# Performance work log

Hardware: AMD Instinct MI355X
Metric: run time of the kernel (lower is better)

The kernel has to match this reference:

```python
import jax, jax.numpy as jnp
import numpy as np

MARGIN = 1.0  # init kwarg
BIG = 1e9     # finite sentinel for masked reductions (dist in [0, 2])


def setup_inputs() -> dict:
    key = jax.random.key(0)
    k1, k2 = jax.random.split(key)
    embeddings = jax.random.normal(k1, (8192, 256), dtype=jnp.float32)
    labels = jax.random.randint(k2, (8192,), 0, 128)
    return {"embeddings": embeddings, "labels": labels}


def reference(embeddings, labels):
    # cosine distance matrix: 1 - x_hat @ x_hat^T, clamped at 0
    norm = jnp.linalg.norm(embeddings, axis=1, keepdims=True)
    x = embeddings / jnp.maximum(norm, 1e-12)  # matches F.normalize eps
    dist = jnp.clip(1.0 - x @ x.T, 0.0, None)  # (B, B)

    same = labels[:, None] == labels[None, :]
    eye = jnp.eye(labels.shape[0], dtype=bool)
    pos_mask = same & ~eye   # same label, different index
    neg_mask = ~same         # different label

    # hard mining: hardest positive (max dist), hardest negative (min dist)
    pos_dist = jnp.max(jnp.where(pos_mask, dist, -BIG), axis=1)  # (B,)
    neg_dist = jnp.min(jnp.where(neg_mask, dist, BIG), axis=1)   # (B,)

    valid = pos_mask.any(axis=1) & neg_mask.any(axis=1)          # (B,)
    per_anchor = jnp.maximum(pos_dist - neg_dist + MARGIN, 0.0)
    loss_sum = jnp.sum(jnp.where(valid, per_anchor, 0.0))
    count = jnp.sum(valid).astype(dist.dtype)
    return jnp.where(count > 0, loss_sum / jnp.maximum(count, 1.0), 0.0)
```

## Files before the change

kernel.cpp:

```cpp
#include <hip/hip_runtime.h>
#include <hip/hip_bf16.h>


constexpr int NB = 8192;
constexpr int NBT = NB / 128;
constexpr int NBLK = NBT * (NBT + 1) / 2;

typedef __attribute__((ext_vector_type(8))) short bf16x8;
typedef __attribute__((ext_vector_type(4))) float f32x4;

typedef __attribute__((address_space(3))) unsigned int lds_u32;
typedef __attribute__((address_space(1))) const unsigned int g_u32;

__device__ inline void load_lds16(const unsigned short* g, unsigned short* l) {
    __builtin_amdgcn_global_load_lds((g_u32*)g, (lds_u32*)l, 16, 0, 0);
}

__device__ inline unsigned short f2bf(float v) {
    __hip_bfloat16 b = __float2bfloat16(v);
    return *reinterpret_cast<unsigned short*>(&b);
}

#define ENC6 0x40C00000u

__global__ __launch_bounds__(256) void norm_kernel(const float* __restrict__ X,
                                                   unsigned short* __restrict__ Xbt,
                                                   unsigned int* minKey,
                                                   unsigned int* maxKey) {
    __shared__ float tile[32][260];
    __shared__ float psum[32][8];
    __shared__ float rscale[32];
    const int t = threadIdx.x;
    const int rb = blockIdx.x * 32;
    const int g = blockIdx.x * 256 + t;
    if (g < NB) { minKey[g] = 0xFFFFFFFFu; maxKey[g] = 0u; }
    #pragma unroll
    for (int k = 0; k < 8; k++) {
        const int f = k * 256 + t;
        const int row = f >> 6, c4 = f & 63;
        const float4 v = *((const float4*)(X + (size_t)(rb + row) * 256) + c4);
        *(float4*)&tile[row][c4 * 4] = v;
    }
    __syncthreads();
    {
        const int r = t >> 3, e = t & 7;
        float s = 0.f;
        #pragma unroll
        for (int i = 0; i < 32; i++) { const float v = tile[r][e * 32 + i]; s += v * v; }
        psum[r][e] = s;
    }
    __syncthreads();
    if (t < 32) {
        float s = 0.f;
        #pragma unroll
        for (int e = 0; e < 8; e++) s += psum[t][e];
        rscale[t] = 1.0f / fmaxf(sqrtf(s), 1e-12f);
    }
    __syncthreads();
    #pragma unroll
    for (int j = 0; j < 4; j++) {
        const int idx = j * 256 + t;
        const int q = idx >> 5, r = idx & 31;
        const float sc = rscale[r];
        unsigned short tmp[8];
        #pragma unroll
        for (int e = 0; e < 8; e++) tmp[e] = f2bf(tile[r][q * 8 + e] * sc);
        *(bf16x8*)(Xbt + ((size_t)q * NB + rb + r) * 8) = *(bf16x8*)tmp;
    }
}

__global__ __launch_bounds__(256) void mine_kernel(
    const unsigned short* __restrict__ Xbt, const int* __restrict__ labels,
    unsigned int* minKey, unsigned int* maxKey) {
    __shared__ unsigned short Bt[32 * 512];
    __shared__ float Lrow[128], Lcol[128];

    const int tb = blockIdx.x;
    int a = (int)((sqrtf(8.0f * (float)tb + 1.0f) - 1.0f) * 0.5f);
    while ((a + 1) * (a + 2) / 2 <= tb) a++;
    while (a * (a + 1) / 2 > tb) a--;
    const int Iblk = tb - a * (a + 1) / 2;
    const int Jblk = a;
    const bool isdiag = (Iblk == Jblk);
    const int Irow0 = Iblk * 128;
    const int Jcol0 = Jblk * 128;

    const int tid = threadIdx.x;
    const int w = tid >> 6;
    const int lane = tid & 63;
    const int quad = lane >> 4;
    const int l16 = lane & 15;
    const int h = w & 1;
    const int v = w >> 1;

    if (tid < 128) Lrow[tid] = (float)labels[Irow0 + tid];
    else Lcol[tid - 128] = (float)labels[Jcol0 + tid - 128];

    f32x4 acc[4][4];
    #pragma unroll
    for (int mi = 0; mi < 4; mi++)
        #pragma unroll
        for (int ni = 0; ni < 4; ni++) acc[mi][ni] = (f32x4){0.f, 0.f, 0.f, 0.f};

    for (int kb = 0; kb < 4; kb++) {
        __syncthreads();
        #pragma unroll
        for (int s = 0; s < 8; s++) {
            const int rg = w * 8 + s;
            const int r2 = rg & 15;
            const int ks = r2 >> 3;
            const int ti = r2 & 7;
            const int base = (rg >> 4) ? Jcol0 : Irow0;
            const int c = kb * 8 + ks * 4 + (lane >> 4);
            const size_t u = (size_t)c * NB + base + ti * 16 + l16;
            load_lds16(Xbt + u * 8, Bt + rg * 512);
        }
        __syncthreads();

        #pragma unroll
        for (int ks = 0; ks < 2; ks++) {
            bf16x8 af[4], bf[4];
            #pragma unroll
            for (int i = 0; i < 4; i++) {
                af[i] = *(const bf16x8*)(Bt + (ks * 8 + h * 4 + i) * 512 + lane * 8);
                bf[i] = *(const bf16x8*)(Bt + (16 + ks * 8 + v * 4 + i) * 512 + lane * 8);
            }
            #pragma unroll
            for (int mi = 0; mi < 4; mi++)
                #pragma unroll
                for (int ni = 0; ni < 4; ni++)
                    acc[mi][ni] = __builtin_amdgcn_mfma_f32_16x16x32_bf16(
                        af[mi], bf[ni], acc[mi][ni], 0, 0, 0);
        }
    }

    const bool diagwave = isdiag && (h == v);
    float flc[4], cMin[4], cMax[4];
    #pragma unroll
    for (int ni = 0; ni < 4; ni++) {
        flc[ni] = Lcol[v * 64 + ni * 16 + l16];
        cMin[ni] = 1e30f;
        cMax[ni] = -1e30f;
    }
    #pragma unroll
    for (int mi = 0; mi < 4; mi++)
        #pragma unroll
        for (int r = 0; r < 4; r++) {
            const float flr = Lrow[h * 64 + mi * 16 + quad * 4 + r];
            float rMin = 1e30f, rMax = -1e30f;
            #pragma unroll
            for (int ni = 0; ni < 4; ni++) {
                const float uu = fminf(fabsf(flr - flc[ni]), 1.0f);
                float key = fmaf(uu, 8.0f, acc[mi][ni][r]);
                if (diagwave && mi == ni)
                    key = (l16 == quad * 4 + r) ? 6.0f : key;
                rMin = fminf(rMin, key);
                rMax = fmaxf(rMax, key);
                cMin[ni] = fminf(cMin[ni], key);
                cMax[ni] = fmaxf(cMax[ni], key);
            }
            #pragma unroll
            for (int m = 1; m <= 8; m <<= 1) {
                rMin = fminf(rMin, __shfl_xor(rMin, m, 64));
                rMax = fmaxf(rMax, __shfl_xor(rMax, m, 64));
            }
            if (l16 == 0) {
                const int row = Irow0 + h * 64 + mi * 16 + quad * 4 + r;
                atomicMin(&minKey[row], __float_as_uint(rMin + 2.0f));
                atomicMax(&maxKey[row], __float_as_uint(rMax + 2.0f));
            }
        }
    if (!isdiag) {
        #pragma unroll
        for (int ni = 0; ni < 4; ni++) {
            float p = cMin[ni], n = cMax[ni];
            p = fminf(p, __shfl_xor(p, 16, 64));
            p = fminf(p, __shfl_xor(p, 32, 64));
            n = fmaxf(n, __shfl_xor(n, 16, 64));
            n = fmaxf(n, __shfl_xor(n, 32, 64));
            if (quad == 0) {
                const int col = Jcol0 + v * 64 + ni * 16 + l16;
                atomicMin(&minKey[col], __float_as_uint(p + 2.0f));
                atomicMax(&maxKey[col], __float_as_uint(n + 2.0f));
            }
        }
    }
}

__global__ __launch_bounds__(1024) void finish_kernel(
    const unsigned int* __restrict__ minKey, const unsigned int* __restrict__ maxKey,
    float* __restrict__ out) {
    const int tid = threadIdx.x;
    float per = 0.f, cnt = 0.f;
    #pragma unroll
    for (int k = 0; k < NB / 1024; k++) {
        const int i = k * 1024 + tid;
        const unsigned int mk = minKey[i], xk = maxKey[i];
        const bool valid = (mk < ENC6) && (xk > ENC6);
        const float ps = __uint_as_float(mk) - 2.0f;
        const float ns = __uint_as_float(xk) - 10.0f;
        const float pd = fmaxf(1.0f - ps, 0.0f);
        const float nd = fmaxf(1.0f - ns, 0.0f);
        per += valid ? fmaxf(pd - nd + 1.0f, 0.0f) : 0.0f;
        cnt += valid ? 1.0f : 0.0f;
    }
    #pragma unroll
    for (int off = 32; off > 0; off >>= 1) {
        per += __shfl_down(per, off, 64);
        cnt += __shfl_down(cnt, off, 64);
    }
    __shared__ float sp[16], sc[16];
    const int wv = tid >> 6, ln = tid & 63;
    if (ln == 0) { sp[wv] = per; sc[wv] = cnt; }
    __syncthreads();
    if (tid == 0) {
        float s = 0.f, c = 0.f;
        #pragma unroll
        for (int i = 0; i < 16; i++) { s += sp[i]; c += sc[i]; }
        out[0] = (c > 0.f) ? s / fmaxf(c, 1.f) : 0.f;
    }
}

extern "C" void kernel_launch(void* const* d_in, const int* in_sizes, int n_in,
                              void* d_out, int out_size, void* d_ws, size_t ws_size,
                              hipStream_t stream) {
    const float* X = (const float*)d_in[0];
    const int* labels = (const int*)d_in[1];
    float* out = (float*)d_out;

    char* ws = (char*)d_ws;
    unsigned short* Xbt = (unsigned short*)ws;
    unsigned int* minKey = (unsigned int*)(ws + (size_t)4 * 1024 * 1024);
    unsigned int* maxKey = minKey + NB;

    norm_kernel<<<NB / 32, 256, 0, stream>>>(X, Xbt, minKey, maxKey);
    mine_kernel<<<NBLK, 256, 0, stream>>>(
        (const unsigned short*)Xbt, labels, minKey, maxKey);
    finish_kernel<<<1, 1024, 0, stream>>>(minKey, maxKey, out);
}
```

Measured before the change: 115.6 us.

## Replace per-row atomic min/max with partial-result buffer and two-stage reduction

Each mine block now writes its per-row and per-column min/max partials into a dense (row x 128 slots) float2 buffer instead of issuing global atomicMin/atomicMax. A new multi-block finish kernel reduces the 128 slots per row, computes the per-anchor loss, and atomically adds into a two-float accumulator, which a tiny final kernel divides. This removes atomic contention on shared row keys, at the cost of an 8 MB partial buffer write/read and an extra kernel launch.

```diff
diff --git a/kernel.cpp b/kernel.cpp
--- a/kernel.cpp
+++ b/kernel.cpp
@@ -21,19 +21,16 @@
     return *reinterpret_cast<unsigned short*>(&b);
 }
 
-#define ENC6 0x40C00000u
 
 __global__ __launch_bounds__(256) void norm_kernel(const float* __restrict__ X,
                                                    unsigned short* __restrict__ Xbt,
-                                                   unsigned int* minKey,
-                                                   unsigned int* maxKey) {
+                                                   float* accum) {
     __shared__ float tile[32][260];
     __shared__ float psum[32][8];
     __shared__ float rscale[32];
     const int t = threadIdx.x;
     const int rb = blockIdx.x * 32;
-    const int g = blockIdx.x * 256 + t;
-    if (g < NB) { minKey[g] = 0xFFFFFFFFu; maxKey[g] = 0u; }
+    if (blockIdx.x == 0 && t == 0) { accum[0] = 0.f; accum[1] = 0.f; }
     #pragma unroll
     for (int k = 0; k < 8; k++) {
         const int f = k * 256 + t;
@@ -71,7 +68,7 @@
 
 __global__ __launch_bounds__(256) void mine_kernel(
     const unsigned short* __restrict__ Xbt, const int* __restrict__ labels,
-    unsigned int* minKey, unsigned int* maxKey) {
+    float2* __restrict__ Part) {
     __shared__ unsigned short Bt[32 * 512];
     __shared__ float Lrow[128], Lcol[128];
 
@@ -166,8 +163,7 @@
             }
             if (l16 == 0) {
                 const int row = Irow0 + h * 64 + mi * 16 + quad * 4 + r;
-                atomicMin(&minKey[row], __float_as_uint(rMin + 2.0f));
-                atomicMax(&maxKey[row], __float_as_uint(rMax + 2.0f));
+                Part[(size_t)row * 128 + (Jblk * 2 + v)] = make_float2(rMin, rMax);
             }
         }
     if (!isdiag) {
@@ -180,45 +176,46 @@
             n = fmaxf(n, __shfl_xor(n, 32, 64));
             if (quad == 0) {
                 const int col = Jcol0 + v * 64 + ni * 16 + l16;
-                atomicMin(&minKey[col], __float_as_uint(p + 2.0f));
-                atomicMax(&maxKey[col], __float_as_uint(n + 2.0f));
-            }
-        }
-    }
-}
-
-__global__ __launch_bounds__(1024) void finish_kernel(
-    const unsigned int* __restrict__ minKey, const unsigned int* __restrict__ maxKey,
-    float* __restrict__ out) {
-    const int tid = threadIdx.x;
-    float per = 0.f, cnt = 0.f;
-    #pragma unroll
-    for (int k = 0; k < NB / 1024; k++) {
-        const int i = k * 1024 + tid;
-        const unsigned int mk = minKey[i], xk = maxKey[i];
-        const bool valid = (mk < ENC6) && (xk > ENC6);
-        const float ps = __uint_as_float(mk) - 2.0f;
-        const float ns = __uint_as_float(xk) - 10.0f;
-        const float pd = fmaxf(1.0f - ps, 0.0f);
-        const float nd = fmaxf(1.0f - ns, 0.0f);
-        per += valid ? fmaxf(pd - nd + 1.0f, 0.0f) : 0.0f;
-        cnt += valid ? 1.0f : 0.0f;
-    }
+                Part[(size_t)col * 128 + (Iblk * 2 + h)] = make_float2(p, n);
+            }
+        }
+    }
+}
+
+__global__ __launch_bounds__(256) void finish1(const float2* __restrict__ Part,
+                                               float* accum) {
+    const int row = blockIdx.x * 256 + threadIdx.x;
+    const float4* p4 = (const float4*)(Part + (size_t)row * 128);
+    float mn = 1e30f, mx = -1e30f;
+    #pragma unroll 8
+    for (int s = 0; s < 64; s++) {
+        const float4 vv = p4[s];
+        mn = fminf(mn, fminf(vv.x, vv.z));
+        mx = fmaxf(mx, fmaxf(vv.y, vv.w));
+    }
+    const bool valid = (mn < 4.0f) && (mx > 6.5f);
+    const float pd = fmaxf(1.0f - mn, 0.0f);
+    const float nd = fmaxf(1.0f - (mx - 8.0f), 0.0f);
+    float per = valid ? fmaxf(pd - nd + 1.0f, 0.0f) : 0.0f;
+    float cnt = valid ? 1.0f : 0.0f;
     #pragma unroll
     for (int off = 32; off > 0; off >>= 1) {
         per += __shfl_down(per, off, 64);
         cnt += __shfl_down(cnt, off, 64);
     }
-    __shared__ float sp[16], sc[16];
-    const int wv = tid >> 6, ln = tid & 63;
+    __shared__ float sp[4], sc[4];
+    const int wv = threadIdx.x >> 6, ln = threadIdx.x & 63;
     if (ln == 0) { sp[wv] = per; sc[wv] = cnt; }
     __syncthreads();
-    if (tid == 0) {
-        float s = 0.f, c = 0.f;
-        #pragma unroll
-        for (int i = 0; i < 16; i++) { s += sp[i]; c += sc[i]; }
-        out[0] = (c > 0.f) ? s / fmaxf(c, 1.f) : 0.f;
-    }
+    if (threadIdx.x == 0) {
+        atomicAdd(&accum[0], sp[0] + sp[1] + sp[2] + sp[3]);
+        atomicAdd(&accum[1], sc[0] + sc[1] + sc[2] + sc[3]);
+    }
+}
+
+__global__ void finish2(const float* __restrict__ accum, float* __restrict__ out) {
+    const float s = accum[0], c = accum[1];
+    out[0] = (c > 0.f) ? s / fmaxf(c, 1.f) : 0.f;
 }
 
 extern "C" void kernel_launch(void* const* d_in, const int* in_sizes, int n_in,
@@ -230,11 +227,12 @@
 
     char* ws = (char*)d_ws;
     unsigned short* Xbt = (unsigned short*)ws;
-    unsigned int* minKey = (unsigned int*)(ws + (size_t)4 * 1024 * 1024);
-    unsigned int* maxKey = minKey + NB;
-
-    norm_kernel<<<NB / 32, 256, 0, stream>>>(X, Xbt, minKey, maxKey);
+    float2* Part = (float2*)(ws + (size_t)4 * 1024 * 1024);
+    float* accum = (float*)(ws + (size_t)12 * 1024 * 1024);
+
+    norm_kernel<<<NB / 32, 256, 0, stream>>>(X, Xbt, accum);
     mine_kernel<<<NBLK, 256, 0, stream>>>(
-        (const unsigned short*)Xbt, labels, minKey, maxKey);
-    finish_kernel<<<1, 1024, 0, stream>>>(minKey, maxKey, out);
-}
+        (const unsigned short*)Xbt, labels, Part);
+    finish1<<<NB / 256, 256, 0, stream>>>(Part, accum);
+    finish2<<<1, 1, 0, stream>>>(accum, out);
+}
```

Result: slower. 121.7 us (+5.3%).
